# Optimization experiments

Measured on AMD Instinct MI355X. Metric: run time of the kernel, lower is better.

## Reference

```python
import jax, jax.numpy as jnp
import numpy as np
import math

N_EMBD = 1024
N_HEAD = 16
B, T = 2, 2048
MASK_VAL = -10.0  # non-standard soft mask value from original module


def setup_inputs() -> dict:
    key = jax.random.key(0)
    k1, k2, k3 = jax.random.split(key, 3)
    scale = 1.0 / math.sqrt(N_EMBD)
    x = jax.random.normal(k1, (B, T, N_EMBD), dtype=jnp.float32)
    # torch Linear weights: (out_features, in_features)
    w_attn = jax.random.normal(k2, (3 * N_EMBD, N_EMBD), dtype=jnp.float32) * scale
    w_proj = jax.random.normal(k3, (N_EMBD, N_EMBD), dtype=jnp.float32) * scale
    return {"x": x, "w_attn": w_attn, "w_proj": w_proj}


def reference(x, w_attn, w_proj):
    Bsz, Tlen, C = x.shape
    hs = C // N_HEAD
    qkv = jnp.einsum('btc,fc->btf', x, w_attn)  # [B,T,3C]
    q, k, v = jnp.split(qkv, 3, axis=-1)
    # [B,H,T,hs]
    q = q.reshape(Bsz, Tlen, N_HEAD, hs).transpose(0, 2, 1, 3)
    k = k.reshape(Bsz, Tlen, N_HEAD, hs).transpose(0, 2, 1, 3)
    v = v.reshape(Bsz, Tlen, N_HEAD, hs).transpose(0, 2, 1, 3)
    att = jnp.einsum('bhqd,bhkd->bhqk', q, k) * (1.0 / math.sqrt(hs))
    causal = jnp.tril(jnp.ones((Tlen, Tlen), dtype=bool))
    att = jnp.where(causal[None, None], att, MASK_VAL)
    att = jax.nn.softmax(att, axis=-1)
    y = jnp.einsum('bhqk,bhkd->bhqd', att, v)
    y = y.transpose(0, 2, 1, 3).reshape(Bsz, Tlen, C)
    return jnp.einsum('btc,fc->btf', y, w_proj)
```

## Files before the change

kernel.cpp:

```cpp
#include <hip/hip_runtime.h>
#include <hip/hip_bf16.h>
#include <stdint.h>

#define BSZ   2
#define TT    2048
#define NH    16
#define HS    64
#define CC    1024
#define C3    3072
#define MT    4096
#define E10   4.5399929762484854e-05f

typedef __bf16 bf16;
typedef __bf16 bf16x8 __attribute__((ext_vector_type(8)));
typedef float  f32x4  __attribute__((ext_vector_type(4)));
typedef short  s16x4  __attribute__((ext_vector_type(4)));

#define AS1 __attribute__((address_space(1)))
#define AS3 __attribute__((address_space(3)))

__device__ __forceinline__ void glds16(const bf16* g, bf16* l) {
    __builtin_amdgcn_global_load_lds((const AS1 void*)g, (AS3 void*)l, 16, 0, 0);
}

__global__ void detect_dtype(const uint16_t* __restrict__ x, int* __restrict__ flag) {
    __shared__ int cnt;
    if (threadIdx.x == 0) cnt = 0;
    __syncthreads();
    int local = 0;
    for (int i = threadIdx.x; i < 512; i += 256) {
        uint16_t u = x[i];
        int e = (u >> 7) & 0xFF;
        if (e >= 96 && e <= 159) local++;
    }
    atomicAdd(&cnt, local);
    __syncthreads();
    if (threadIdx.x == 0) *flag = (cnt >= 461) ? 0 : 1;
}

#define NX8  (MT * CC / 8)
#define NWA8 (C3 * CC / 8)
#define NWP8 (CC * CC / 8)
__global__ __launch_bounds__(256)
void convert_all(const float* __restrict__ x, const float* __restrict__ wa,
                 const float* __restrict__ wp, bf16* __restrict__ xd,
                 bf16* __restrict__ wad, bf16* __restrict__ wpd,
                 const int* __restrict__ flag) {
    if (*flag == 0) return;
    long i = (long)blockIdx.x * 256 + threadIdx.x;
    const float* s; bf16* d; long off;
    if (i < NX8)             { s = x;  d = xd;  off = i; }
    else if (i < NX8 + NWA8) { s = wa; d = wad; off = i - NX8; }
    else                     { s = wp; d = wpd; off = i - NX8 - NWA8; }
    const float4* sp = reinterpret_cast<const float4*>(s) + off * 2;
    float4 a = sp[0], b = sp[1];
    bf16x8 r;
    r[0] = (bf16)a.x; r[1] = (bf16)a.y; r[2] = (bf16)a.z; r[3] = (bf16)a.w;
    r[4] = (bf16)b.x; r[5] = (bf16)b.y; r[6] = (bf16)b.z; r[7] = (bf16)b.w;
    reinterpret_cast<bf16x8*>(d)[off] = r;
}

__global__ __launch_bounds__(256)
void gemm_bt(const bf16* __restrict__ A0, const bf16* __restrict__ A1,
             const bf16* __restrict__ B0, const bf16* __restrict__ B1,
             void* __restrict__ C, const int* __restrict__ flag,
             int M, int N, int K, int lda, int ldb, int ldc, int cf32_dyn) {
    __shared__ bf16 As[2][128 * 32];
    __shared__ bf16 Bs[2][128 * 32];

    const int f = *flag;
    const bf16* A = f ? A1 : A0;
    const bf16* B = f ? B1 : B0;
    const int cf32 = cf32_dyn & f;

    const int tid  = threadIdx.x;
    const int lane = tid & 63;
    const int wave = tid >> 6;
    const int wm   = wave >> 1;
    const int wn   = wave & 1;
    const int quad = lane >> 4;
    const int l16  = lane & 15;

    const int row0 = blockIdx.y * 128;
    const int col0 = blockIdx.x * 128;

    const int srow = tid >> 2;
    const int skk  = (tid & 3) * 8;

    const bf16* Ap = A + (long)(row0 + srow) * lda + skk;
    const bf16* Bp = B + (long)(col0 + srow) * ldb + skk;

    auto stage = [&](int k0, int buf) {
        glds16(Ap + k0,                  &As[buf][wave * 512]);
        glds16(Ap + (long)64 * lda + k0, &As[buf][wave * 512 + 2048]);
        glds16(Bp + k0,                  &Bs[buf][wave * 512]);
        glds16(Bp + (long)64 * ldb + k0, &Bs[buf][wave * 512 + 2048]);
    };

    f32x4 acc[4][4] = {};
    stage(0, 0);

    for (int k0 = 0; k0 < K; k0 += 32) {
        const int buf = (k0 >> 5) & 1;
        __syncthreads();
        if (k0 + 32 < K) stage(k0 + 32, buf ^ 1);

        const bf16* Ac = As[buf];
        const bf16* Bc = Bs[buf];
        bf16x8 af[4], bfv[4];
#pragma unroll
        for (int mi = 0; mi < 4; ++mi)
            af[mi] = *reinterpret_cast<const bf16x8*>(&Ac[(wm * 64 + mi * 16 + l16) * 32 + quad * 8]);
#pragma unroll
        for (int ni = 0; ni < 4; ++ni)
            bfv[ni] = *reinterpret_cast<const bf16x8*>(&Bc[(wn * 64 + ni * 16 + l16) * 32 + quad * 8]);
#pragma unroll
        for (int mi = 0; mi < 4; ++mi)
#pragma unroll
            for (int ni = 0; ni < 4; ++ni)
                acc[mi][ni] = __builtin_amdgcn_mfma_f32_16x16x32_bf16(af[mi], bfv[ni], acc[mi][ni], 0, 0, 0);
    }

#pragma unroll
    for (int mi = 0; mi < 4; ++mi)
#pragma unroll
        for (int ni = 0; ni < 4; ++ni)
#pragma unroll
            for (int r = 0; r < 4; ++r) {
                int row = row0 + wm * 64 + mi * 16 + quad * 4 + r;
                int col = col0 + wn * 64 + ni * 16 + l16;
                float v = acc[mi][ni][r];
                if (cf32) ((float*)C)[(long)row * ldc + col] = v;
                else      ((bf16*)C)[(long)row * ldc + col] = (bf16)v;
            }
}

__global__ __launch_bounds__(256)
void gemm_bt64(const bf16* __restrict__ A0, const bf16* __restrict__ A1,
               const bf16* __restrict__ B0, const bf16* __restrict__ B1,
               void* __restrict__ C, const int* __restrict__ flag,
               int M, int N, int K, int lda, int ldb, int ldc, int cf32_dyn) {
    __shared__ bf16 As[2][128 * 32];
    __shared__ bf16 Bs[2][64 * 32];

    const int f = *flag;
    const bf16* A = f ? A1 : A0;
    const bf16* B = f ? B1 : B0;
    const int cf32 = cf32_dyn & f;

    const int tid  = threadIdx.x;
    const int lane = tid & 63;
    const int wave = tid >> 6;
    const int wm   = wave >> 1;
    const int wn   = wave & 1;
    const int quad = lane >> 4;
    const int l16  = lane & 15;

    const int row0 = blockIdx.y * 128;
    const int col0 = blockIdx.x * 64;

    const int srow = tid >> 2;
    const int skk  = (tid & 3) * 8;

    const bf16* Ap = A + (long)(row0 + srow) * lda + skk;
    const bf16* Bp = B + (long)(col0 + srow) * ldb + skk;

    auto stage = [&](int k0, int buf) {
        glds16(Ap + k0,                  &As[buf][wave * 512]);
        glds16(Ap + (long)64 * lda + k0, &As[buf][wave * 512 + 2048]);
        glds16(Bp + k0,                  &Bs[buf][wave * 512]);
    };

    f32x4 acc[4][2] = {};
    stage(0, 0);

    for (int k0 = 0; k0 < K; k0 += 32) {
        const int buf = (k0 >> 5) & 1;
        __syncthreads();
        if (k0 + 32 < K) stage(k0 + 32, buf ^ 1);

        const bf16* Ac = As[buf];
        const bf16* Bc = Bs[buf];
        bf16x8 af[4], bfv[2];
#pragma unroll
        for (int mi = 0; mi < 4; ++mi)
            af[mi] = *reinterpret_cast<const bf16x8*>(&Ac[(wm * 64 + mi * 16 + l16) * 32 + quad * 8]);
#pragma unroll
        for (int ni = 0; ni < 2; ++ni)
            bfv[ni] = *reinterpret_cast<const bf16x8*>(&Bc[(wn * 32 + ni * 16 + l16) * 32 + quad * 8]);
#pragma unroll
        for (int mi = 0; mi < 4; ++mi)
#pragma unroll
            for (int ni = 0; ni < 2; ++ni)
                acc[mi][ni] = __builtin_amdgcn_mfma_f32_16x16x32_bf16(af[mi], bfv[ni], acc[mi][ni], 0, 0, 0);
    }

#pragma unroll
    for (int mi = 0; mi < 4; ++mi)
#pragma unroll
        for (int ni = 0; ni < 2; ++ni)
#pragma unroll
            for (int r = 0; r < 4; ++r) {
                int row = row0 + wm * 64 + mi * 16 + quad * 4 + r;
                int col = col0 + wn * 32 + ni * 16 + l16;
                float v = acc[mi][ni][r];
                if (cf32) ((float*)C)[(long)row * ldc + col] = v;
                else      ((bf16*)C)[(long)row * ldc + col] = (bf16)v;
            }
}

__global__ __launch_bounds__(256)
void vtranspose(const bf16* __restrict__ qkv, bf16* __restrict__ Vt,
                float* __restrict__ Vtile) {
    __shared__ bf16 Vl[64 * 72];
    const int tc = blockIdx.x, bh = blockIdx.y;
    const int b = bh >> 4, h = bh & 15;
    const int tid = threadIdx.x;
    const int row = tid >> 2, doff = (tid & 3) * 16;
    const bf16* src = qkv + ((long)b * TT + tc * 64 + row) * C3 + 2 * CC + h * 64 + doff;
    *reinterpret_cast<bf16x8*>(&Vl[row * 72 + doff])     = *reinterpret_cast<const bf16x8*>(src);
    *reinterpret_cast<bf16x8*>(&Vl[row * 72 + doff + 8]) = *reinterpret_cast<const bf16x8*>(src + 8);
    __syncthreads();
    const int d = tid >> 2, poff = (tid & 3) * 16;
    bf16 tmp[16];
    float s = 0.f;
#pragma unroll
    for (int i = 0; i < 16; ++i) {
        int pos = poff + i;
        int tl = ((pos & 12) << 2) | ((pos & 48) >> 2) | (pos & 3);
        tmp[i] = Vl[tl * 72 + d];
        s += (float)tmp[i];
    }
    bf16* dst = Vt + ((long)bh * 64 + d) * 2048 + tc * 64 + poff;
    *reinterpret_cast<bf16x8*>(dst)     = *reinterpret_cast<bf16x8*>(tmp);
    *reinterpret_cast<bf16x8*>(dst + 8) = *reinterpret_cast<bf16x8*>(tmp + 8);
    s += __shfl_xor(s, 1, 64);
    s += __shfl_xor(s, 2, 64);
    if ((tid & 3) == 0)
        Vtile[((long)bh * 32 + tc) * 64 + d] = s;
}

__global__ void vts_suffix(const float* __restrict__ Vtile, float* __restrict__ Vts) {
    const int bh = blockIdx.x, d = threadIdx.x;
    Vts[((long)bh * 33 + 32) * 64 + d] = 0.f;
    float acc = 0.f;
    for (int kt = 31; kt >= 0; --kt) {
        acc += Vtile[((long)bh * 32 + kt) * 64 + d];
        Vts[((long)bh * 33 + kt) * 64 + d] = acc;
    }
}

__global__ __launch_bounds__(256)
void attn(bf16* __restrict__ qkv, const bf16* __restrict__ Vt,
          const float* __restrict__ Vts) {
    __shared__ bf16 Ks[2][64 * 64];
    __shared__ bf16 Vs[2][64 * 64];

    const int tid  = threadIdx.x;
    const int lane = tid & 63;
    const int wave = tid >> 6;
    const int quad = lane >> 4;
    const int l16  = lane & 15;

    const int f2   = blockIdx.x;
    const int xcd  = f2 & 7;
    const int slot = f2 >> 3;
    const int bh   = (slot & 3) * 8 + xcd;
    const int chunk = 31 - (slot >> 2);
    const int b = bh >> 4, h = bh & 15;
    const int q0 = chunk * 64;
    const long rbase = (long)b * TT;

    const bf16* qp = qkv + (rbase + q0 + wave * 16 + l16) * C3 + h * HS;
    bf16x8 qf0 = *reinterpret_cast<const bf16x8*>(qp + quad * 8);
    bf16x8 qf1 = *reinterpret_cast<const bf16x8*>(qp + 32 + quad * 8);

    f32x4 O[4] = {};
    float lp = 0.f;

    const int rl  = lane >> 3;
    const int cs  = (lane & 7) ^ rl;
    const int row0dma = wave * 16 + rl;
    const bf16* kgb = qkv + (rbase + row0dma) * C3 + CC + h * HS + cs * 8;
    const bf16* vgb = Vt + ((long)(b * NH + h) * 64 + row0dma) * 2048 + cs * 8;
    const int sx = l16 & 7;

    auto stage = [&](int kt, int buf) {
        glds16(kgb + (long)(kt * 64) * C3,     &Ks[buf][wave * 1024]);
        glds16(kgb + (long)(kt * 64 + 8) * C3, &Ks[buf][wave * 1024 + 512]);
        glds16(vgb + kt * 64,                  &Vs[buf][wave * 1024]);
        glds16(vgb + 8 * 2048 + kt * 64,       &Vs[buf][wave * 1024 + 512]);
    };

    const int ktend = chunk + 1;
    stage(0, 0);

    for (int kt = 0; kt < ktend; ++kt) {
        const int buf = kt & 1;
        __syncthreads();
        if (kt + 1 < ktend) stage(kt + 1, buf ^ 1);

        const bf16* Kc = Ks[buf];
        const bf16* Vc = Vs[buf];

        bf16x8 kf0[4], kf1[4];
#pragma unroll
        for (int g = 0; g < 4; ++g) {
            const int krow = g * 16 + l16;
            kf0[g] = *reinterpret_cast<const bf16x8*>(&Kc[krow * 64 + ((quad ^ sx) * 8)]);
            kf1[g] = *reinterpret_cast<const bf16x8*>(&Kc[krow * 64 + (((4 + quad) ^ sx) * 8)]);
        }
        s16x4 vf[4][4];
#pragma unroll
        for (int dg = 0; dg < 4; ++dg) {
            const int vrow = dg * 16 + l16;
            union { uint4 u; s16x4 s[2]; } ua, ub;
            ua.u = *reinterpret_cast<const uint4*>(&Vc[vrow * 64 + (((2 * quad) ^ sx) * 8)]);
            ub.u = *reinterpret_cast<const uint4*>(&Vc[vrow * 64 + (((2 * quad + 1) ^ sx) * 8)]);
            vf[dg][0] = ua.s[0]; vf[dg][1] = ua.s[1];
            vf[dg][2] = ub.s[0]; vf[dg][3] = ub.s[1];
        }

        f32x4 S[4] = {};
#pragma unroll
        for (int g = 0; g < 4; ++g) {
            S[g] = __builtin_amdgcn_mfma_f32_16x16x32_bf16(kf0[g], qf0, S[g], 0, 0, 0);
            S[g] = __builtin_amdgcn_mfma_f32_16x16x32_bf16(kf1[g], qf1, S[g], 0, 0, 0);
        }

        const bool dtile = (kt == chunk);
        const int ql = wave * 16 + l16;
        s16x4 pk[4];
#pragma unroll
        for (int g = 0; g < 4; ++g) {
#pragma unroll
            for (int r = 0; r < 4; ++r) {
                float p = __expf(S[g][r] * 0.125f);
                if (dtile) {
                    int kl = g * 16 + quad * 4 + r;
                    p = (kl > ql) ? E10 : p;
                }
                lp += p;
                union { bf16 b_; short s_; } u;
                u.b_ = (bf16)p;
                pk[g][r] = u.s_;
            }
        }

#pragma unroll
        for (int dg = 0; dg < 4; ++dg) {
            O[dg] = __builtin_amdgcn_mfma_f32_16x16x16bf16_1k(vf[dg][0], pk[0], O[dg], 0, 0, 0);
            O[dg] = __builtin_amdgcn_mfma_f32_16x16x16bf16_1k(vf[dg][1], pk[1], O[dg], 0, 0, 0);
            O[dg] = __builtin_amdgcn_mfma_f32_16x16x16bf16_1k(vf[dg][2], pk[2], O[dg], 0, 0, 0);
            O[dg] = __builtin_amdgcn_mfma_f32_16x16x16bf16_1k(vf[dg][3], pk[3], O[dg], 0, 0, 0);
        }
    }

    lp += __shfl_xor(lp, 16, 64);
    lp += __shfl_xor(lp, 32, 64);

    const int nfut = TT - ktend * 64;
    const float l = lp + (float)nfut * E10;
    const float invl = 1.0f / l;
    const float* vfp = Vts + ((long)(b * NH + h) * 33 + ktend) * 64;

    bf16* yp = qkv + (rbase + q0 + wave * 16 + l16) * C3 + h * HS;
#pragma unroll
    for (int dg = 0; dg < 4; ++dg) {
        bf16 outv[4];
#pragma unroll
        for (int r = 0; r < 4; ++r) {
            float o = O[dg][r] + E10 * vfp[dg * 16 + quad * 4 + r];
            outv[r] = (bf16)(o * invl);
        }
        *reinterpret_cast<uint2*>(yp + dg * 16 + quad * 4) =
            *reinterpret_cast<uint2*>(outv);
    }
}

extern "C" void kernel_launch(void* const* d_in, const int* in_sizes, int n_in,
                              void* d_out, int out_size, void* d_ws, size_t ws_size,
                              hipStream_t stream) {
    const void* x      = d_in[0];
    const void* w_attn = d_in[1];
    const void* w_proj = d_in[2];

    char* ws = (char*)d_ws;
    bf16*  qkv    = (bf16*)ws;
    int*   flag   = (int*)(ws + (size_t)MT * C3 * 2);
    float* Vts    = (float*)(ws + (size_t)MT * C3 * 2 + 256);
    bf16*  wp_cvt = (bf16*)((char*)Vts + 32 * 33 * 64 * 4);
    float* Vtile  = (float*)((char*)wp_cvt + (size_t)CC * CC * 2);

    bf16* x_cvt  = (bf16*)d_out;
    bf16* wa_cvt = (bf16*)d_out + (size_t)MT * CC;
    bf16* Vtg    = (bf16*)d_out;

    detect_dtype<<<1, 256, 0, stream>>>((const uint16_t*)x, flag);
    convert_all<<<(NX8 + NWA8 + NWP8) / 256, 256, 0, stream>>>(
        (const float*)x, (const float*)w_attn, (const float*)w_proj,
        x_cvt, wa_cvt, wp_cvt, flag);

    gemm_bt<<<dim3(C3 / 128, MT / 128), 256, 0, stream>>>(
        (const bf16*)x, x_cvt, (const bf16*)w_attn, wa_cvt, qkv, flag,
        MT, C3, CC, CC, CC, C3, 0);

    vtranspose<<<dim3(32, BSZ * NH), 256, 0, stream>>>(qkv, Vtg, Vtile);
    vts_suffix<<<dim3(BSZ * NH), dim3(64), 0, stream>>>(Vtile, Vts);

    attn<<<dim3(1024), 256, 0, stream>>>(qkv, Vtg, Vts);

    gemm_bt64<<<dim3(CC / 64, MT / 128), 256, 0, stream>>>(
        qkv, qkv, (const bf16*)w_proj, wp_cvt, d_out, flag,
        MT, CC, CC, C3, CC, CC, 1);
}
```

Measured before the change: 183.7 us.

## Fuse V transpose into QKV GEMM epilogue and use exp2 in softmax

The QKV GEMM epilogue now writes the V columns directly in the transposed, permuted layout the attention kernel expects. This removes the separate vtranspose pass, which is replaced by a lighter kernel that only computes the per-tile V sums. Q and K are stored in a narrower 2048-column buffer, and the projection GEMM reads attention output with the new stride. The softmax exponent also switches from expf with a 0.125 scale to exp2f with a prescaled constant. The V epilogue writes 8-byte strided chunks, which may coalesce worse than the previous row-major stores.

```diff
diff --git a/kernel.cpp b/kernel.cpp
--- a/kernel.cpp
+++ b/kernel.cpp
@@ -10,6 +10,7 @@
 #define C3    3072
 #define MT    4096
 #define E10   4.5399929762484854e-05f
+#define SCL2  0.1803368801111204f
 
 typedef __bf16 bf16;
 typedef __bf16 bf16x8 __attribute__((ext_vector_type(8)));
@@ -63,8 +64,10 @@
 __global__ __launch_bounds__(256)
 void gemm_bt(const bf16* __restrict__ A0, const bf16* __restrict__ A1,
              const bf16* __restrict__ B0, const bf16* __restrict__ B1,
-             void* __restrict__ C, const int* __restrict__ flag,
-             int M, int N, int K, int lda, int ldb, int ldc, int cf32_dyn) {
+             void* __restrict__ Cmain, bf16* __restrict__ Cv,
+             const int* __restrict__ flag,
+             int M, int N, int K, int lda, int ldb, int ldc,
+             int split_col, int cf32_dyn) {
     __shared__ bf16 As[2][128 * 32];
     __shared__ bf16 Bs[2][128 * 32];
 
@@ -121,18 +124,36 @@
                 acc[mi][ni] = __builtin_amdgcn_mfma_f32_16x16x32_bf16(af[mi], bfv[ni], acc[mi][ni], 0, 0, 0);
     }
 
-#pragma unroll
-    for (int mi = 0; mi < 4; ++mi)
-#pragma unroll
-        for (int ni = 0; ni < 4; ++ni)
-#pragma unroll
-            for (int r = 0; r < 4; ++r) {
-                int row = row0 + wm * 64 + mi * 16 + quad * 4 + r;
-                int col = col0 + wn * 64 + ni * 16 + l16;
-                float v = acc[mi][ni][r];
-                if (cf32) ((float*)C)[(long)row * ldc + col] = v;
-                else      ((bf16*)C)[(long)row * ldc + col] = (bf16)v;
+    if (split_col < 0 || col0 < split_col) {
+#pragma unroll
+        for (int mi = 0; mi < 4; ++mi)
+#pragma unroll
+            for (int ni = 0; ni < 4; ++ni)
+#pragma unroll
+                for (int r = 0; r < 4; ++r) {
+                    int row = row0 + wm * 64 + mi * 16 + quad * 4 + r;
+                    int col = col0 + wn * 64 + ni * 16 + l16;
+                    float v = acc[mi][ni][r];
+                    if (cf32) ((float*)Cmain)[(long)row * ldc + col] = v;
+                    else      ((bf16*)Cmain)[(long)row * ldc + col] = (bf16)v;
+                }
+    } else {
+        const int h  = (col0 - split_col + wn * 64) >> 6;
+        const int bq = row0 >> 11;
+        const int tc = ((row0 & 2047) >> 6) + wm;
+#pragma unroll
+        for (int ni = 0; ni < 4; ++ni) {
+            long vrow = (long)(bq * NH + h) * 64 + ni * 16 + l16;
+#pragma unroll
+            for (int mi = 0; mi < 4; ++mi) {
+                bf16 outv[4];
+#pragma unroll
+                for (int r = 0; r < 4; ++r) outv[r] = (bf16)acc[mi][ni][r];
+                *reinterpret_cast<uint2*>(&Cv[vrow * 2048 + tc * 64 + quad * 16 + mi * 4]) =
+                    *reinterpret_cast<uint2*>(outv);
             }
+        }
+    }
 }
 
 __global__ __launch_bounds__(256)
@@ -210,34 +231,21 @@
 }
 
 __global__ __launch_bounds__(256)
-void vtranspose(const bf16* __restrict__ qkv, bf16* __restrict__ Vt,
-                float* __restrict__ Vtile) {
-    __shared__ bf16 Vl[64 * 72];
-    const int tc = blockIdx.x, bh = blockIdx.y;
-    const int b = bh >> 4, h = bh & 15;
+void vtile2(const bf16* __restrict__ Vt, float* __restrict__ Vtile) {
+    const int kt = blockIdx.x, bh = blockIdx.y;
     const int tid = threadIdx.x;
-    const int row = tid >> 2, doff = (tid & 3) * 16;
-    const bf16* src = qkv + ((long)b * TT + tc * 64 + row) * C3 + 2 * CC + h * 64 + doff;
-    *reinterpret_cast<bf16x8*>(&Vl[row * 72 + doff])     = *reinterpret_cast<const bf16x8*>(src);
-    *reinterpret_cast<bf16x8*>(&Vl[row * 72 + doff + 8]) = *reinterpret_cast<const bf16x8*>(src + 8);
-    __syncthreads();
-    const int d = tid >> 2, poff = (tid & 3) * 16;
-    bf16 tmp[16];
+    const int d = tid >> 2, part = tid & 3;
+    const bf16* p = Vt + ((long)bh * 64 + d) * 2048 + kt * 64 + part * 16;
     float s = 0.f;
 #pragma unroll
-    for (int i = 0; i < 16; ++i) {
-        int pos = poff + i;
-        int tl = ((pos & 12) << 2) | ((pos & 48) >> 2) | (pos & 3);
-        tmp[i] = Vl[tl * 72 + d];
-        s += (float)tmp[i];
-    }
-    bf16* dst = Vt + ((long)bh * 64 + d) * 2048 + tc * 64 + poff;
-    *reinterpret_cast<bf16x8*>(dst)     = *reinterpret_cast<bf16x8*>(tmp);
-    *reinterpret_cast<bf16x8*>(dst + 8) = *reinterpret_cast<bf16x8*>(tmp + 8);
+    for (int i = 0; i < 2; ++i) {
+        bf16x8 v = *reinterpret_cast<const bf16x8*>(p + i * 8);
+#pragma unroll
+        for (int j = 0; j < 8; ++j) s += (float)v[j];
+    }
     s += __shfl_xor(s, 1, 64);
     s += __shfl_xor(s, 2, 64);
-    if ((tid & 3) == 0)
-        Vtile[((long)bh * 32 + tc) * 64 + d] = s;
+    if (part == 0) Vtile[((long)bh * 32 + kt) * 64 + d] = s;
 }
 
 __global__ void vts_suffix(const float* __restrict__ Vtile, float* __restrict__ Vts) {
@@ -251,7 +259,7 @@
 }
 
 __global__ __launch_bounds__(256)
-void attn(bf16* __restrict__ qkv, const bf16* __restrict__ Vt,
+void attn(bf16* __restrict__ qk, const bf16* __restrict__ Vt,
           const float* __restrict__ Vts) {
     __shared__ bf16 Ks[2][64 * 64];
     __shared__ bf16 Vs[2][64 * 64];
@@ -271,7 +279,7 @@
     const int q0 = chunk * 64;
     const long rbase = (long)b * TT;
 
-    const bf16* qp = qkv + (rbase + q0 + wave * 16 + l16) * C3 + h * HS;
+    const bf16* qp = qk + (rbase + q0 + wave * 16 + l16) * 2048 + h * HS;
     bf16x8 qf0 = *reinterpret_cast<const bf16x8*>(qp + quad * 8);
     bf16x8 qf1 = *reinterpret_cast<const bf16x8*>(qp + 32 + quad * 8);
 
@@ -281,15 +289,15 @@
     const int rl  = lane >> 3;
     const int cs  = (lane & 7) ^ rl;
     const int row0dma = wave * 16 + rl;
-    const bf16* kgb = qkv + (rbase + row0dma) * C3 + CC + h * HS + cs * 8;
+    const bf16* kgb = qk + (rbase + row0dma) * 2048 + CC + h * HS + cs * 8;
     const bf16* vgb = Vt + ((long)(b * NH + h) * 64 + row0dma) * 2048 + cs * 8;
     const int sx = l16 & 7;
 
     auto stage = [&](int kt, int buf) {
-        glds16(kgb + (long)(kt * 64) * C3,     &Ks[buf][wave * 1024]);
-        glds16(kgb + (long)(kt * 64 + 8) * C3, &Ks[buf][wave * 1024 + 512]);
-        glds16(vgb + kt * 64,                  &Vs[buf][wave * 1024]);
-        glds16(vgb + 8 * 2048 + kt * 64,       &Vs[buf][wave * 1024 + 512]);
+        glds16(kgb + (long)(kt * 64) * 2048,     &Ks[buf][wave * 1024]);
+        glds16(kgb + (long)(kt * 64 + 8) * 2048, &Ks[buf][wave * 1024 + 512]);
+        glds16(vgb + kt * 64,                    &Vs[buf][wave * 1024]);
+        glds16(vgb + 8 * 2048 + kt * 64,         &Vs[buf][wave * 1024 + 512]);
     };
 
     const int ktend = chunk + 1;
@@ -335,7 +343,7 @@
         for (int g = 0; g < 4; ++g) {
 #pragma unroll
             for (int r = 0; r < 4; ++r) {
-                float p = __expf(S[g][r] * 0.125f);
+                float p = __builtin_exp2f(S[g][r] * SCL2);
                 if (dtile) {
                     int kl = g * 16 + quad * 4 + r;
                     p = (kl > ql) ? E10 : p;
@@ -364,7 +372,7 @@
     const float invl = 1.0f / l;
     const float* vfp = Vts + ((long)(b * NH + h) * 33 + ktend) * 64;
 
-    bf16* yp = qkv + (rbase + q0 + wave * 16 + l16) * C3 + h * HS;
+    bf16* yp = qk + (rbase + q0 + wave * 16 + l16) * 2048 + h * HS;
 #pragma unroll
     for (int dg = 0; dg < 4; ++dg) {
         bf16 outv[4];
@@ -386,15 +394,16 @@
     const void* w_proj = d_in[2];
 
     char* ws = (char*)d_ws;
-    bf16*  qkv    = (bf16*)ws;
-    int*   flag   = (int*)(ws + (size_t)MT * C3 * 2);
-    float* Vts    = (float*)(ws + (size_t)MT * C3 * 2 + 256);
-    bf16*  wp_cvt = (bf16*)((char*)Vts + 32 * 33 * 64 * 4);
+    bf16*  qk     = (bf16*)ws;
+    bf16*  Vt     = (bf16*)(ws + (size_t)MT * 2048 * 2);
+    char*  p2     = ws + (size_t)MT * 2048 * 2 + (size_t)32 * 64 * 2048 * 2;
+    int*   flag   = (int*)p2;
+    float* Vts    = (float*)(p2 + 256);
+    bf16*  wp_cvt = (bf16*)(p2 + 256 + 32 * 33 * 64 * 4);
     float* Vtile  = (float*)((char*)wp_cvt + (size_t)CC * CC * 2);
 
     bf16* x_cvt  = (bf16*)d_out;
     bf16* wa_cvt = (bf16*)d_out + (size_t)MT * CC;
-    bf16* Vtg    = (bf16*)d_out;
 
     detect_dtype<<<1, 256, 0, stream>>>((const uint16_t*)x, flag);
     convert_all<<<(NX8 + NWA8 + NWP8) / 256, 256, 0, stream>>>(
@@ -402,15 +411,15 @@
         x_cvt, wa_cvt, wp_cvt, flag);
 
     gemm_bt<<<dim3(C3 / 128, MT / 128), 256, 0, stream>>>(
-        (const bf16*)x, x_cvt, (const bf16*)w_attn, wa_cvt, qkv, flag,
-        MT, C3, CC, CC, CC, C3, 0);
-
-    vtranspose<<<dim3(32, BSZ * NH), 256, 0, stream>>>(qkv, Vtg, Vtile);
+        (const bf16*)x, x_cvt, (const bf16*)w_attn, wa_cvt, qk, Vt, flag,
+        MT, C3, CC, CC, CC, 2048, 2048, 0);
+
+    vtile2<<<dim3(32, BSZ * NH), 256, 0, stream>>>(Vt, Vtile);
     vts_suffix<<<dim3(BSZ * NH), dim3(64), 0, stream>>>(Vtile, Vts);
 
-    attn<<<dim3(1024), 256, 0, stream>>>(qkv, Vtg, Vts);
+    attn<<<dim3(1024), 256, 0, stream>>>(qk, Vt, Vts);
 
     gemm_bt64<<<dim3(CC / 64, MT / 128), 256, 0, stream>>>(
-        qkv, qkv, (const bf16*)w_proj, wp_cvt, d_out, flag,
-        MT, CC, CC, C3, CC, CC, 1);
-}
+        qk, qk, (const bf16*)w_proj, wp_cvt, d_out, flag,
+        MT, CC, CC, 2048, CC, CC, 1);
+}
```

After: 181.5 us. Within noise of the previous version (-1.2%).
